# Performance work log

Measured on AMD Instinct MI355X. Metric: run time of the kernel, lower is better.

Reference implementation:

```python
import jax, jax.numpy as jnp
import numpy as np

TEMP = 0.5  # matches temperature init kwarg
EPS = 1e-12  # F.normalize eps


def _l2norm(x):
    # F.normalize(x, dim=1): x / max(||x||, eps)
    n = jnp.linalg.norm(x, axis=1, keepdims=True)
    return x / jnp.maximum(n, EPS)


def setup_inputs() -> dict:
    key = jax.random.key(0)
    k1, k2 = jax.random.split(key)
    B, D = 4096, 256
    return {
        "x_i": jax.random.normal(k1, (B, D), dtype=jnp.float32),
        "x_j": jax.random.normal(k2, (B, D), dtype=jnp.float32),
    }


def reference(x_i, x_j):
    B = x_i.shape[0]
    z = jnp.concatenate([_l2norm(x_i), _l2norm(x_j)], axis=0)  # [2B, D]
    # cosine similarity of normalized rows == matmul (avoids NxNxD broadcast)
    sim = (z @ z.T) / TEMP  # [2B, 2B]
    idx = jnp.arange(B)
    # diagonals at offsets +B and -B = positive pairs
    pos = jnp.concatenate([sim[idx, idx + B], sim[idx + B, idx]])  # [2B]
    exp_sim = jnp.exp(sim)
    # neg = all off-diagonal entries per row (neg_mask = ~eye(2B))
    exp_neg = exp_sim.sum(axis=1) - jnp.exp(jnp.diagonal(sim))  # [2B]
    exp_pos = jnp.exp(pos)
    loss = -jnp.log(exp_pos / (exp_pos + exp_neg))
    return loss.mean()
```

## Files before the change

kernel.cpp:

```cpp
#include <hip/hip_runtime.h>
#include <hip/hip_bf16.h>

typedef __attribute__((ext_vector_type(8))) int   i32x8;
typedef __attribute__((ext_vector_type(4))) int   i32x4;
typedef __attribute__((ext_vector_type(4))) float f32x4;

constexpr int BB = 4096;
constexpr int D  = 256;
constexpr int R2 = 8192;
constexpr int NSPLIT = 32;
constexpr int CT = 64;
constexpr int NT = (R2 / NSPLIT) / CT;
constexpr float SQRT2 = 1.41421356237309515f;
constexpr float E2 = 7.38905609893065f;

__device__ __forceinline__ void async16(const unsigned char* g, unsigned char* l) {
    __builtin_amdgcn_global_load_lds(
        (const __attribute__((address_space(1))) void*)g,
        (__attribute__((address_space(3))) void*)l,
        16, 0, 0);
}

#define MFMA8(A, B, C) \
    __builtin_amdgcn_mfma_scale_f32_16x16x128_f8f6f4((A), (B), (C), 0, 0, 0, 127, 0, 127)

__global__ __launch_bounds__(256) void norm_kernel(const float* __restrict__ xi,
                                                   const float* __restrict__ xj,
                                                   int* __restrict__ z8,
                                                   float* __restrict__ pos,
                                                   float* __restrict__ out) {
    const int wid = threadIdx.x >> 6, lane = threadIdx.x & 63;
    const int k = blockIdx.x * 4 + wid;
    if (blockIdx.x == 0 && threadIdx.x == 0) out[0] = 0.f;
    const float4* a4 = reinterpret_cast<const float4*>(xi + (size_t)k * D);
    const float4* b4 = reinterpret_cast<const float4*>(xj + (size_t)k * D);
    float4 a = a4[lane], b = b4[lane];
    float ssi = a.x*a.x + a.y*a.y + a.z*a.z + a.w*a.w;
    float ssj = b.x*b.x + b.y*b.y + b.z*b.z + b.w*b.w;
    float dot = a.x*b.x + a.y*b.y + a.z*b.z + a.w*b.w;
#pragma unroll
    for (int off = 32; off; off >>= 1) {
        ssi += __shfl_xor(ssi, off);
        ssj += __shfl_xor(ssj, off);
        dot += __shfl_xor(dot, off);
    }
    const float inv_i = 1.0f / fmaxf(sqrtf(ssi), 1e-12f);
    const float inv_j = 1.0f / fmaxf(sqrtf(ssj), 1e-12f);
    const float si = inv_i * SQRT2, sj = inv_j * SQRT2;
    int pi = __builtin_amdgcn_cvt_pk_fp8_f32(a.x*si, a.y*si, 0, false);
    pi     = __builtin_amdgcn_cvt_pk_fp8_f32(a.z*si, a.w*si, pi, true);
    int pj = __builtin_amdgcn_cvt_pk_fp8_f32(b.x*sj, b.y*sj, 0, false);
    pj     = __builtin_amdgcn_cvt_pk_fp8_f32(b.z*sj, b.w*sj, pj, true);
    z8[(size_t)k * 64 + lane]        = pi;
    z8[(size_t)(k + BB) * 64 + lane] = pj;
    if (lane == 0) pos[k] = dot * inv_i * inv_j * 2.0f;
}

__global__ __launch_bounds__(256) void sim_kernel(const unsigned char* __restrict__ z8,
                                                  float* __restrict__ partial) {
    __shared__ unsigned char tb[2][CT * D];
    const int tid = threadIdx.x;
    const int wid = tid >> 6, lane = tid & 63;
    const int lrow = lane & 15, quad = lane >> 4;
    const int r0 = blockIdx.x * 128 + wid * 32;
    const int cbase = blockIdx.y * (R2 / NSPLIT);

    const int srow = tid >> 4;
    const unsigned char* gstage = z8 + (size_t)(cbase + srow) * D + ((tid & 15) ^ srow) * 16;

    async16(gstage + 0*4096, &tb[0][0*4096 + wid*1024]);
    async16(gstage + 1*4096, &tb[0][1*4096 + wid*1024]);
    async16(gstage + 2*4096, &tb[0][2*4096 + wid*1024]);
    async16(gstage + 3*4096, &tb[0][3*4096 + wid*1024]);

    const unsigned char* abase = z8 + (size_t)(r0 + lrow) * D + quad * 32;
    const i32x8 a0k0 = *reinterpret_cast<const i32x8*>(abase + 0*4096      );
    const i32x8 a0k1 = *reinterpret_cast<const i32x8*>(abase + 0*4096 + 128);
    const i32x8 a1k0 = *reinterpret_cast<const i32x8*>(abase + 1*4096      );
    const i32x8 a1k1 = *reinterpret_cast<const i32x8*>(abase + 1*4096 + 128);

    f32x4 racc0 = {0.f,0.f,0.f,0.f}, racc1 = {0.f,0.f,0.f,0.f};

    __syncthreads();

    for (int ct = 0; ct < NT; ++ct) {
        const unsigned char* tbb = tb[ct & 1];
        if (ct + 1 < NT) {
            const unsigned char* gs = gstage + (size_t)(ct + 1) * (CT * D);
            unsigned char* dn = &tb[(ct + 1) & 1][wid * 1024];
            async16(gs + 0*4096, dn + 0*4096);
            async16(gs + 1*4096, dn + 1*4096);
            async16(gs + 2*4096, dn + 2*4096);
            async16(gs + 3*4096, dn + 3*4096);
        }
#pragma unroll
        for (int n = 0; n < 4; ++n) {
            const unsigned char* rbp = tbb + (n*16 + lrow) * D;
            const int pe0 = (quad*2) ^ lrow;
            const int pe1 = (8 + quad*2) ^ lrow;
            const i32x4 lo0 = *reinterpret_cast<const i32x4*>(rbp + pe0*16);
            const i32x4 hi0 = *reinterpret_cast<const i32x4*>(rbp + (pe0^1)*16);
            const i32x4 lo1 = *reinterpret_cast<const i32x4*>(rbp + pe1*16);
            const i32x4 hi1 = *reinterpret_cast<const i32x4*>(rbp + (pe1^1)*16);
            const i32x8 b0 = __builtin_shufflevector(lo0, hi0, 0,1,2,3,4,5,6,7);
            const i32x8 b1 = __builtin_shufflevector(lo1, hi1, 0,1,2,3,4,5,6,7);

            f32x4 c0 = {0.f,0.f,0.f,0.f}, c1 = {0.f,0.f,0.f,0.f};
            c0 = MFMA8(a0k0, b0, c0);  c0 = MFMA8(a0k1, b1, c0);
            c1 = MFMA8(a1k0, b0, c1);  c1 = MFMA8(a1k1, b1, c1);

            racc0[0] += __expf(c0[0]); racc0[1] += __expf(c0[1]);
            racc0[2] += __expf(c0[2]); racc0[3] += __expf(c0[3]);
            racc1[0] += __expf(c1[0]); racc1[1] += __expf(c1[1]);
            racc1[2] += __expf(c1[2]); racc1[3] += __expf(c1[3]);
        }
        __syncthreads();
    }

#define REDUCE_STORE(RV, M)                                                     \
    {                                                                           \
        _Pragma("unroll")                                                       \
        for (int j = 0; j < 4; ++j) {                                           \
            float v = (RV)[j];                                                  \
            v += __shfl_xor(v, 1);                                              \
            v += __shfl_xor(v, 2);                                              \
            v += __shfl_xor(v, 4);                                              \
            v += __shfl_xor(v, 8);                                              \
            if (lrow == 0)                                                      \
                partial[(size_t)blockIdx.y * R2 + r0 + (M)*16 + quad*4 + j] = v;\
        }                                                                       \
    }
    REDUCE_STORE(racc0, 0)
    REDUCE_STORE(racc1, 1)
#undef REDUCE_STORE
}

__global__ __launch_bounds__(256) void reduce_kernel(const float* __restrict__ partial,
                                                     const float* __restrict__ pos,
                                                     float* __restrict__ out) {
    __shared__ float wsum[4];
    const int tid = threadIdx.x;
    const int r = blockIdx.x * 256 + tid;
    float S = 0.f;
#pragma unroll
    for (int s = 0; s < NSPLIT; ++s) S += partial[(size_t)s * R2 + r];
    const float p = pos[r & (BB - 1)];
    float lsum = __logf(__expf(p) + S - E2) - p;
#pragma unroll
    for (int off = 32; off; off >>= 1) lsum += __shfl_xor(lsum, off);
    if ((tid & 63) == 0) wsum[tid >> 6] = lsum;
    __syncthreads();
    if (tid == 0) {
        float t = wsum[0] + wsum[1] + wsum[2] + wsum[3];
        atomicAdd(out, t * (1.0f / (float)R2));
    }
}

extern "C" void kernel_launch(void* const* d_in, const int* in_sizes, int n_in,
                              void* d_out, int out_size, void* d_ws, size_t ws_size,
                              hipStream_t stream) {
    (void)in_sizes; (void)n_in; (void)out_size; (void)ws_size;
    const float* xi = (const float*)d_in[0];
    const float* xj = (const float*)d_in[1];
    float* out = (float*)d_out;

    unsigned char* z8 = (unsigned char*)d_ws;
    float* partial = (float*)((char*)d_ws + (size_t)R2 * D);
    float* pos     = (float*)((char*)d_ws + (size_t)R2 * D + (size_t)NSPLIT*R2*4);

    norm_kernel<<<BB / 4, 256, 0, stream>>>(xi, xj, (int*)z8, pos, out);
    sim_kernel<<<dim3(R2 / 128, NSPLIT), 256, 0, stream>>>(z8, partial);
    reduce_kernel<<<NSPLIT, 256, 0, stream>>>(partial, pos, out);
}
```

Measured before the change: 91.38 us.

## Load similarity B tiles straight from global and fold log2e into the fp8 scale

The similarity kernel no longer stages column tiles through double-buffered LDS with async global-to-LDS copies and block barriers. Each wave now loads its B fragments directly from global memory, with a one-step register prefetch. The normalization scale now includes log2(e), so the exponent sum can use the hardware exp2 and skip a multiply per element. The column split is halved to 16, giving each block more work, and the reduce grid is written in terms of R2. The cost is that the four waves each re-read the same B rows through the caches. The last prefetch also reads past the z8 buffer into other workspace memory.

```diff
diff --git a/kernel.cpp b/kernel.cpp
--- a/kernel.cpp
+++ b/kernel.cpp
@@ -2,24 +2,15 @@
 #include <hip/hip_bf16.h>
 
 typedef __attribute__((ext_vector_type(8))) int   i32x8;
-typedef __attribute__((ext_vector_type(4))) int   i32x4;
 typedef __attribute__((ext_vector_type(4))) float f32x4;
 
 constexpr int BB = 4096;
 constexpr int D  = 256;
 constexpr int R2 = 8192;
-constexpr int NSPLIT = 32;
-constexpr int CT = 64;
-constexpr int NT = (R2 / NSPLIT) / CT;
-constexpr float SQRT2 = 1.41421356237309515f;
+constexpr int NSPLIT = 16;
+constexpr int NG = (R2 / NSPLIT) / 16;
+constexpr float SCALE = 1.6986436005760381f;
 constexpr float E2 = 7.38905609893065f;
-
-__device__ __forceinline__ void async16(const unsigned char* g, unsigned char* l) {
-    __builtin_amdgcn_global_load_lds(
-        (const __attribute__((address_space(1))) void*)g,
-        (__attribute__((address_space(3))) void*)l,
-        16, 0, 0);
-}
 
 #define MFMA8(A, B, C) \
     __builtin_amdgcn_mfma_scale_f32_16x16x128_f8f6f4((A), (B), (C), 0, 0, 0, 127, 0, 127)
@@ -46,7 +37,7 @@
     }
     const float inv_i = 1.0f / fmaxf(sqrtf(ssi), 1e-12f);
     const float inv_j = 1.0f / fmaxf(sqrtf(ssj), 1e-12f);
-    const float si = inv_i * SQRT2, sj = inv_j * SQRT2;
+    const float si = inv_i * SCALE, sj = inv_j * SCALE;
     int pi = __builtin_amdgcn_cvt_pk_fp8_f32(a.x*si, a.y*si, 0, false);
     pi     = __builtin_amdgcn_cvt_pk_fp8_f32(a.z*si, a.w*si, pi, true);
     int pj = __builtin_amdgcn_cvt_pk_fp8_f32(b.x*sj, b.y*sj, 0, false);
@@ -58,63 +49,42 @@
 
 __global__ __launch_bounds__(256) void sim_kernel(const unsigned char* __restrict__ z8,
                                                   float* __restrict__ partial) {
-    __shared__ unsigned char tb[2][CT * D];
     const int tid = threadIdx.x;
     const int wid = tid >> 6, lane = tid & 63;
     const int lrow = lane & 15, quad = lane >> 4;
     const int r0 = blockIdx.x * 128 + wid * 32;
     const int cbase = blockIdx.y * (R2 / NSPLIT);
 
-    const int srow = tid >> 4;
-    const unsigned char* gstage = z8 + (size_t)(cbase + srow) * D + ((tid & 15) ^ srow) * 16;
-
-    async16(gstage + 0*4096, &tb[0][0*4096 + wid*1024]);
-    async16(gstage + 1*4096, &tb[0][1*4096 + wid*1024]);
-    async16(gstage + 2*4096, &tb[0][2*4096 + wid*1024]);
-    async16(gstage + 3*4096, &tb[0][3*4096 + wid*1024]);
-
     const unsigned char* abase = z8 + (size_t)(r0 + lrow) * D + quad * 32;
-    const i32x8 a0k0 = *reinterpret_cast<const i32x8*>(abase + 0*4096      );
-    const i32x8 a0k1 = *reinterpret_cast<const i32x8*>(abase + 0*4096 + 128);
-    const i32x8 a1k0 = *reinterpret_cast<const i32x8*>(abase + 1*4096      );
-    const i32x8 a1k1 = *reinterpret_cast<const i32x8*>(abase + 1*4096 + 128);
+    const i32x8 a0k0 = *reinterpret_cast<const i32x8*>(abase            );
+    const i32x8 a0k1 = *reinterpret_cast<const i32x8*>(abase       + 128);
+    const i32x8 a1k0 = *reinterpret_cast<const i32x8*>(abase + 16*D      );
+    const i32x8 a1k1 = *reinterpret_cast<const i32x8*>(abase + 16*D + 128);
 
     f32x4 racc0 = {0.f,0.f,0.f,0.f}, racc1 = {0.f,0.f,0.f,0.f};
 
-    __syncthreads();
+    const unsigned char* bp = z8 + (size_t)(cbase + lrow) * D + quad * 32;
+    i32x8 nb0 = *reinterpret_cast<const i32x8*>(bp      );
+    i32x8 nb1 = *reinterpret_cast<const i32x8*>(bp + 128);
 
-    for (int ct = 0; ct < NT; ++ct) {
-        const unsigned char* tbb = tb[ct & 1];
-        if (ct + 1 < NT) {
-            const unsigned char* gs = gstage + (size_t)(ct + 1) * (CT * D);
-            unsigned char* dn = &tb[(ct + 1) & 1][wid * 1024];
-            async16(gs + 0*4096, dn + 0*4096);
-            async16(gs + 1*4096, dn + 1*4096);
-            async16(gs + 2*4096, dn + 2*4096);
-            async16(gs + 3*4096, dn + 3*4096);
-        }
-#pragma unroll
-        for (int n = 0; n < 4; ++n) {
-            const unsigned char* rbp = tbb + (n*16 + lrow) * D;
-            const int pe0 = (quad*2) ^ lrow;
-            const int pe1 = (8 + quad*2) ^ lrow;
-            const i32x4 lo0 = *reinterpret_cast<const i32x4*>(rbp + pe0*16);
-            const i32x4 hi0 = *reinterpret_cast<const i32x4*>(rbp + (pe0^1)*16);
-            const i32x4 lo1 = *reinterpret_cast<const i32x4*>(rbp + pe1*16);
-            const i32x4 hi1 = *reinterpret_cast<const i32x4*>(rbp + (pe1^1)*16);
-            const i32x8 b0 = __builtin_shufflevector(lo0, hi0, 0,1,2,3,4,5,6,7);
-            const i32x8 b1 = __builtin_shufflevector(lo1, hi1, 0,1,2,3,4,5,6,7);
+    for (int g = 0; g < NG; ++g) {
+        const i32x8 b0 = nb0, b1 = nb1;
+        bp += 16 * D;
+        nb0 = *reinterpret_cast<const i32x8*>(bp      );
+        nb1 = *reinterpret_cast<const i32x8*>(bp + 128);
 
-            f32x4 c0 = {0.f,0.f,0.f,0.f}, c1 = {0.f,0.f,0.f,0.f};
-            c0 = MFMA8(a0k0, b0, c0);  c0 = MFMA8(a0k1, b1, c0);
-            c1 = MFMA8(a1k0, b0, c1);  c1 = MFMA8(a1k1, b1, c1);
+        f32x4 c0 = {0.f,0.f,0.f,0.f}, c1 = {0.f,0.f,0.f,0.f};
+        c0 = MFMA8(a0k0, b0, c0);  c0 = MFMA8(a0k1, b1, c0);
+        c1 = MFMA8(a1k0, b0, c1);  c1 = MFMA8(a1k1, b1, c1);
 
-            racc0[0] += __expf(c0[0]); racc0[1] += __expf(c0[1]);
-            racc0[2] += __expf(c0[2]); racc0[3] += __expf(c0[3]);
-            racc1[0] += __expf(c1[0]); racc1[1] += __expf(c1[1]);
-            racc1[2] += __expf(c1[2]); racc1[3] += __expf(c1[3]);
-        }
-        __syncthreads();
+        racc0[0] += __builtin_amdgcn_exp2f(c0[0]);
+        racc0[1] += __builtin_amdgcn_exp2f(c0[1]);
+        racc0[2] += __builtin_amdgcn_exp2f(c0[2]);
+        racc0[3] += __builtin_amdgcn_exp2f(c0[3]);
+        racc1[0] += __builtin_amdgcn_exp2f(c1[0]);
+        racc1[1] += __builtin_amdgcn_exp2f(c1[1]);
+        racc1[2] += __builtin_amdgcn_exp2f(c1[2]);
+        racc1[3] += __builtin_amdgcn_exp2f(c1[3]);
     }
 
 #define REDUCE_STORE(RV, M)                                                     \
@@ -170,5 +140,5 @@
 
     norm_kernel<<<BB / 4, 256, 0, stream>>>(xi, xj, (int*)z8, pos, out);
     sim_kernel<<<dim3(R2 / 128, NSPLIT), 256, 0, stream>>>(z8, partial);
-    reduce_kernel<<<NSPLIT, 256, 0, stream>>>(partial, pos, out);
+    reduce_kernel<<<R2 / 256, 256, 0, stream>>>(partial, pos, out);
 }
```

After: 125.5 us. 1.37x slower.
